# Performance work log

Hardware: AMD Instinct MI355X
Metric: run time of the kernel (lower is better)

## Reference

```python
import jax, jax.numpy as jnp
import numpy as np

N_NODES = 50000
N_EDGES = 600000
N_GRAPHS = 256
D = 128          # hidden_dim
L = 4            # num_layer
OUT = 1          # output_dim
ATOM_DIMS = [119, 5, 12, 12, 10, 6, 6, 2, 2]   # table size = dim+1, pad to 120
BOND_DIMS = [6, 6, 2, 2, 2]                    # table size = dim+1, pad to 7
BN_EPS = 1e-5


def setup_inputs() -> dict:
    key = jax.random.key(0)
    ks = jax.random.split(key, 16)
    x = jax.random.randint(ks[0], (N_NODES, 9), 0, 3)
    edge_index = jax.random.randint(ks[1], (2, N_EDGES), 0, N_NODES)
    edge_attr = jax.random.randint(ks[2], (N_EDGES, 5), 0, 3)
    batch = jnp.sort(jax.random.randint(ks[3], (N_NODES,), 0, N_GRAPHS))
    s = 0.1
    # padded atom embedding tables: [9, 120, D] (rows beyond dim+1 unused)
    atom_emb = jax.random.normal(ks[4], (9, 120, D), jnp.float32) * s
    # padded bond tables per layer: [L, 5, 7, D]
    bond_emb = jax.random.normal(ks[5], (L, 5, 7, D), jnp.float32) * s
    lin_w = jax.random.normal(ks[6], (L, D, D), jnp.float32) * (1.0 / np.sqrt(D))
    lin_b = jnp.zeros((L, D), jnp.float32)
    bn_gamma = jnp.ones((L, D), jnp.float32)
    bn_beta = jnp.zeros((L, D), jnp.float32)
    mlp_w1 = jax.random.normal(ks[7], (D // 2, D), jnp.float32) * (1.0 / np.sqrt(D))
    mlp_b1 = jnp.zeros((D // 2,), jnp.float32)
    mlp_w2 = jax.random.normal(ks[8], (OUT, D // 2), jnp.float32) * (1.0 / np.sqrt(D // 2))
    mlp_b2 = jnp.zeros((OUT,), jnp.float32)
    return dict(x=x, edge_index=edge_index, edge_attr=edge_attr, batch=batch,
                atom_emb=atom_emb, bond_emb=bond_emb, lin_w=lin_w, lin_b=lin_b,
                bn_gamma=bn_gamma, bn_beta=bn_beta,
                mlp_w1=mlp_w1, mlp_b1=mlp_b1, mlp_w2=mlp_w2, mlp_b2=mlp_b2)


def _multi_embed(tables, idx):
    # tables: [F, V, D], idx: [N, F] -> sum_f tables[f][idx[:, f]]
    return jax.vmap(lambda t, i: t[i], in_axes=(0, 1))(tables, idx).sum(0)


def reference(x, edge_index, edge_attr, batch, atom_emb, bond_emb, lin_w, lin_b,
              bn_gamma, bn_beta, mlp_w1, mlp_b1, mlp_w2, mlp_b2):
    n = x.shape[0]
    loop = jnp.arange(n, dtype=edge_index.dtype)
    src = jnp.concatenate([edge_index[0], loop])           # x_j (source)
    dst = jnp.concatenate([edge_index[1], loop])           # aggregate into target i
    ea = jnp.concatenate([edge_attr, jnp.zeros((n, 5), edge_attr.dtype)], axis=0)
    h = _multi_embed(atom_emb, x)                          # [N, D]
    for l in range(L):
        e_emb = _multi_embed(bond_emb[l], ea)              # [E+N, D]
        msg = h[src] + e_emb                               # gather + add
        aggr = jax.ops.segment_sum(msg, dst, num_segments=n)
        z = aggr @ lin_w[l].T + lin_b[l]
        mu = z.mean(0)
        var = z.var(0)                                     # biased, matches torch BN fwd
        h = jax.nn.relu((z - mu) * jax.lax.rsqrt(var + BN_EPS) * bn_gamma[l] + bn_beta[l])
    # global mean pool
    sums = jax.ops.segment_sum(h, batch, num_segments=N_GRAPHS)
    cnt = jax.ops.segment_sum(jnp.ones((n,), h.dtype), batch, num_segments=N_GRAPHS)
    g = sums / jnp.maximum(cnt, 1.0)[:, None]
    # MLP head (dropout inactive at inference)
    out = jax.nn.relu(g @ mlp_w1.T + mlp_b1) @ mlp_w2.T + mlp_b2
    return out
```

## Files before the change

### kernel.cpp

```cpp
#include <hip/hip_runtime.h>
#include <hip/hip_bf16.h>
#include <stdint.h>

#define D 128
#define NGRAPH 256
#define BN_EPS 1e-5f
#define NCOMBO 243
#define AGG_BLOCKS 512
#define AGG_THREADS 768
#define MAXDEG 48
#define GEMM_ROWS 128

typedef unsigned short u16;
typedef __attribute__((ext_vector_type(8))) short bf16x8;
typedef __attribute__((ext_vector_type(4))) float f32x4;

__device__ inline u16 f2bf(float a) {
  return __builtin_bit_cast(u16, __float2bfloat16(a));
}
__device__ inline uint32_t pk2(float a, float b) {
  return (uint32_t)f2bf(a) | ((uint32_t)f2bf(b) << 16);
}
__device__ inline float bflo(uint32_t u) { return __builtin_bit_cast(float, u << 16); }
__device__ inline float bfhi(uint32_t u) { return __builtin_bit_cast(float, u & 0xffff0000u); }
__device__ inline void unpack8(uint4 v, float* f) {
  f[0] = bflo(v.x); f[1] = bfhi(v.x); f[2] = bflo(v.y); f[3] = bfhi(v.y);
  f[4] = bflo(v.z); f[5] = bfhi(v.z); f[6] = bflo(v.w); f[7] = bfhi(v.w);
}

__global__ __launch_bounds__(256) void setup_kernel(
    const int* __restrict__ x, const float* __restrict__ atom_emb,
    float* __restrict__ h0,
    const int* __restrict__ src, const int* __restrict__ dst,
    const int* __restrict__ attr, int* __restrict__ deg,
    uint2* __restrict__ edges, int ne,
    const int* __restrict__ batch, int* __restrict__ goff,
    float* __restrict__ gsum, int n) {
  int b = blockIdx.x, tid = threadIdx.x;
  int nscat = (ne + 255) >> 8;
  int nemb = (n * 32 + 255) >> 8;
  if (b < nscat) {
    int e = b * 256 + tid;
    if (e >= ne) return;
    int d = dst[e];
    int slot = atomicAdd(&deg[d], 1);
    if (slot >= MAXDEG) return;
    int a0 = attr[e * 5 + 0], a1 = attr[e * 5 + 1], a2 = attr[e * 5 + 2];
    int a3 = attr[e * 5 + 3], a4 = attr[e * 5 + 4];
    uint32_t packed = (uint32_t)(a0 * 81 + a1 * 27 + a2 * 9 + a3 * 3 + a4);
    uint2 r; r.x = (uint32_t)src[e]; r.y = packed;
    edges[(size_t)d * MAXDEG + slot] = r;
  } else if (b < nscat + nemb) {
    int t = (b - nscat) * 256 + tid;
    int node = t >> 5, cq = t & 31;
    if (node >= n) return;
    float4 acc = {0.f, 0.f, 0.f, 0.f};
#pragma unroll
    for (int f = 0; f < 9; f++) {
      int idx = x[node * 9 + f];
      const float4* row = (const float4*)(atom_emb + ((size_t)f * 120 + idx) * D);
      float4 v = row[cq];
      acc.x += v.x; acc.y += v.y; acc.z += v.z; acc.w += v.w;
    }
    ((float4*)(h0 + (size_t)node * D))[cq] = acc;
  } else {
    if (b == nscat + nemb) {
      for (int t = tid; t < 4 * 2 * D; t += 256) gsum[t] = 0.f;
    }
    int i = (b - nscat - nemb) * 256 + tid;
    if (i >= n) return;
    int bb = batch[i];
    if (i == 0) {
      for (int g = 0; g <= bb; g++) goff[g] = 0;
    } else {
      int pb = batch[i - 1];
      for (int g = pb + 1; g <= bb; g++) goff[g] = i;
    }
    if (i == n - 1) {
      for (int g = bb + 1; g <= NGRAPH; g++) goff[g] = n;
    }
  }
}

__global__ __launch_bounds__(128) void prep_kernel(
    const float* __restrict__ bemb, const float* __restrict__ linw,
    u16* __restrict__ tabB, u16* __restrict__ wball) {
  __shared__ float row[D];
  int b = blockIdx.x, c = threadIdx.x;
  if (b < 4 * NCOMBO) {
    int l = b / NCOMBO, r = b % NCOMBO;
    const float* bond = bemb + (size_t)l * 5 * 7 * D;
    const float* W = linw + (size_t)l * D * D;
    int a0 = r / 81, a1 = (r / 27) % 3, a2 = (r / 9) % 3, a3 = (r / 3) % 3,
        a4 = r % 3;
    float v = bond[(0 * 7 + a0) * D + c] + bond[(1 * 7 + a1) * D + c] +
              bond[(2 * 7 + a2) * D + c] + bond[(3 * 7 + a3) * D + c] +
              bond[(4 * 7 + a4) * D + c];
    row[c] = v;
    __syncthreads();
    float s = 0.f;
    for (int k = 0; k < D; k++) s += row[k] * W[(size_t)c * D + k];
    tabB[((size_t)l * NCOMBO + r) * D + c] = f2bf(s);
  } else {
    int i = b - 4 * NCOMBO;
    int l = i >> 7, j = i & 127;
    float v = linw[(size_t)l * D * D + (size_t)j * D + c];
    wball[(size_t)l * D * D + (size_t)j * D + (c ^ ((j & 7) << 3))] = f2bf(v);
  }
}

__global__ __launch_bounds__(256) void gemm_kernel(const float* __restrict__ in,
                                                   const u16* __restrict__ Wb,
                                                   const float* __restrict__ gsum,
                                                   const float* __restrict__ gamma,
                                                   const float* __restrict__ beta,
                                                   float invN,
                                                   u16* __restrict__ out, int M) {
  __shared__ u16 wlds[D * D];
  __shared__ float bns[2 * D];
  int tid = threadIdx.x;
  for (int i = tid; i < D * D / 8; i += 256)
    ((uint4*)wlds)[i] = ((const uint4*)Wb)[i];
  if (gsum && tid < D) {
    float s = gsum[tid], q = gsum[D + tid];
    float mu = s * invN;
    float var = q * invN - mu * mu;
    float sc = rsqrtf(var + BN_EPS) * gamma[tid];
    bns[tid] = sc;
    bns[D + tid] = beta[tid] - mu * sc;
  }
  __syncthreads();

  int wave = tid >> 6, lane = tid & 63;
  int quad = lane >> 4, l16 = lane & 15;
  int m0 = blockIdx.x * GEMM_ROWS + wave * 32;

  f32x4 acc[2][8];
#pragma unroll
  for (int mt = 0; mt < 2; mt++)
#pragma unroll
    for (int t = 0; t < 8; t++) acc[mt][t] = (f32x4){0.f, 0.f, 0.f, 0.f};

#pragma unroll
  for (int kk = 0; kk < 4; kk++) {
    int k0 = kk * 32 + quad * 8;
    bf16x8 a[2];
#pragma unroll
    for (int mt = 0; mt < 2; mt++) {
      int m = m0 + mt * 16 + l16;
      if (m < M) {
        float4 v0 = *(const float4*)(in + (size_t)m * D + k0);
        float4 v1 = *(const float4*)(in + (size_t)m * D + k0 + 4);
        if (gsum) {
          float4 sc0 = *(const float4*)(bns + k0);
          float4 sc1 = *(const float4*)(bns + k0 + 4);
          float4 sh0 = *(const float4*)(bns + D + k0);
          float4 sh1 = *(const float4*)(bns + D + k0 + 4);
          v0.x = fmaxf(v0.x * sc0.x + sh0.x, 0.f);
          v0.y = fmaxf(v0.y * sc0.y + sh0.y, 0.f);
          v0.z = fmaxf(v0.z * sc0.z + sh0.z, 0.f);
          v0.w = fmaxf(v0.w * sc0.w + sh0.w, 0.f);
          v1.x = fmaxf(v1.x * sc1.x + sh1.x, 0.f);
          v1.y = fmaxf(v1.y * sc1.y + sh1.y, 0.f);
          v1.z = fmaxf(v1.z * sc1.z + sh1.z, 0.f);
          v1.w = fmaxf(v1.w * sc1.w + sh1.w, 0.f);
        }
        uint4 pa = {pk2(v0.x, v0.y), pk2(v0.z, v0.w), pk2(v1.x, v1.y), pk2(v1.z, v1.w)};
        a[mt] = __builtin_bit_cast(bf16x8, pa);
      } else {
        uint4 pz = {0u, 0u, 0u, 0u};
        a[mt] = __builtin_bit_cast(bf16x8, pz);
      }
    }
#pragma unroll
    for (int nt = 0; nt < 8; nt++) {
      int nrow = nt * 16 + l16;
      uint4 braw = *(const uint4*)(wlds + nrow * D + (k0 ^ ((nrow & 7) << 3)));
      bf16x8 bfrag = __builtin_bit_cast(bf16x8, braw);
      acc[0][nt] = __builtin_amdgcn_mfma_f32_16x16x32_bf16(a[0], bfrag, acc[0][nt], 0, 0, 0);
      acc[1][nt] = __builtin_amdgcn_mfma_f32_16x16x32_bf16(a[1], bfrag, acc[1][nt], 0, 0, 0);
    }
  }
#pragma unroll
  for (int mt = 0; mt < 2; mt++)
#pragma unroll
    for (int r = 0; r < 4; r++) {
      int row = m0 + mt * 16 + quad * 4 + r;
      if (row < M) {
#pragma unroll
        for (int nt = 0; nt < 8; nt++)
          out[(size_t)row * D + nt * 16 + l16] = f2bf(acc[mt][nt][r]);
      }
    }
}

__global__ __launch_bounds__(AGG_THREADS, 6) void agg_kernel(
    const u16* __restrict__ ht, const u16* __restrict__ tabT,
    const float* __restrict__ linb, const uint2* __restrict__ edges,
    const int* __restrict__ deg, float* __restrict__ z,
    float* __restrict__ gsum, int n) {
  __shared__ u16 tabs[NCOMBO * D];
  __shared__ float psum[2 * D];
  int tid = threadIdx.x;
  for (int i = tid; i < NCOMBO * D / 8; i += AGG_THREADS)
    ((uint4*)tabs)[i] = ((const uint4*)tabT)[i];
  if (tid < 2 * D) psum[tid] = 0.f;
  __syncthreads();

  int lane = tid & 63;
  int g = lane >> 4;
  int c8 = lane & 15;
  int wid = (blockIdx.x * AGG_THREADS + tid) >> 6;
  int nw = (gridDim.x * AGG_THREADS) >> 6;

  float lbz[8];
  {
    float4 l0 = ((const float4*)linb)[c8 * 2];
    float4 l1 = ((const float4*)linb)[c8 * 2 + 1];
    float t0[8];
    unpack8(*(const uint4*)(tabs + c8 * 8), t0);
    lbz[0] = l0.x + t0[0]; lbz[1] = l0.y + t0[1];
    lbz[2] = l0.z + t0[2]; lbz[3] = l0.w + t0[3];
    lbz[4] = l1.x + t0[4]; lbz[5] = l1.y + t0[5];
    lbz[6] = l1.z + t0[6]; lbz[7] = l1.w + t0[7];
  }
  float st[8];
#pragma unroll
  for (int i = 0; i < 8; i++) st[i] = 0.f;

  int dgv = (wid < n) ? deg[wid] : 0;
  for (int node = wid; node < n; node += nw) {
    int dg = dgv;
    if (node + nw < n) dgv = deg[node + nw];
    int cnt = (dg > MAXDEG) ? MAXDEG : dg;
    int base = node * MAXDEG;
    int e = base + cnt;
    int j = base + g;

    uint4 selfv;
    if (g == 0) selfv = *(const uint4*)(ht + (size_t)node * D + c8 * 8);
    bool v0 = j < e, v1 = j + 4 < e, v2 = j + 8 < e;
    uint2 rA, rB, rC;
    if (v0) rA = edges[j];
    if (v1) rB = edges[j + 4];
    if (v2) rC = edges[j + 8];
    uint4 hA, hB;
    if (v0) hA = *(const uint4*)(ht + (size_t)rA.x * D + c8 * 8);
    if (v1) hB = *(const uint4*)(ht + (size_t)rB.x * D + c8 * 8);

    float acc[8];
#pragma unroll
    for (int i = 0; i < 8; i++) acc[i] = 0.f;

    while (v0) {
      bool v3 = j + 12 < e;
      uint2 rN;
      if (v3) rN = edges[j + 12];
      uint4 hC;
      if (v2) hC = *(const uint4*)(ht + (size_t)rC.x * D + c8 * 8);
      uint4 tb = *(const uint4*)(tabs + (size_t)rA.y * D + c8 * 8);
      float hf[8], tf[8];
      unpack8(hA, hf);
      unpack8(tb, tf);
#pragma unroll
      for (int i = 0; i < 8; i++) acc[i] += hf[i] + tf[i];
      rA = rB; rB = rC; rC = rN;
      hA = hB; hB = hC;
      v0 = v1; v1 = v2; v2 = v3;
      j += 4;
    }

    if (g == 0) {
      float sv[8];
      unpack8(selfv, sv);
#pragma unroll
      for (int i = 0; i < 8; i++) acc[i] += sv[i] + lbz[i];
    }

#pragma unroll
    for (int off = 16; off <= 32; off <<= 1)
#pragma unroll
      for (int i = 0; i < 8; i++) acc[i] += __shfl_xor(acc[i], off, 64);

    if (g == 0) {
      float4 za = {acc[0], acc[1], acc[2], acc[3]};
      float4 zb4 = {acc[4], acc[5], acc[6], acc[7]};
      float4* zr = (float4*)(z + (size_t)node * D);
      zr[c8 * 2] = za;
      zr[c8 * 2 + 1] = zb4;
    } else if (g == 1) {
#pragma unroll
      for (int i = 0; i < 8; i++) st[i] += acc[i];
    } else if (g == 2) {
#pragma unroll
      for (int i = 0; i < 8; i++) st[i] += acc[i] * acc[i];
    }
  }
  {
    int c0 = c8 * 8;
    if (g == 1) {
#pragma unroll
      for (int i = 0; i < 8; i++) atomicAdd(&psum[c0 + i], st[i]);
    } else if (g == 2) {
#pragma unroll
      for (int i = 0; i < 8; i++) atomicAdd(&psum[D + c0 + i], st[i]);
    }
  }
  __syncthreads();
  if (tid < 2 * D) atomicAdd(&gsum[tid], psum[tid]);
}

__global__ __launch_bounds__(512) void poolmlp_kernel(
    const float* __restrict__ z, const float* __restrict__ gsum,
    const float* __restrict__ gamma, const float* __restrict__ beta,
    float invN, const int* __restrict__ goff,
    const float* __restrict__ w1, const float* __restrict__ b1,
    const float* __restrict__ w2, const float* __restrict__ b2,
    float* __restrict__ out) {
  __shared__ float sdata[512];
  __shared__ float pg[D];
  int g = blockIdx.x;
  int c = threadIdx.x & 127, r4 = threadIdx.x >> 7;
  float s0 = gsum[c], q0 = gsum[D + c];
  float mu = s0 * invN;
  float var = q0 * invN - mu * mu;
  float sc = rsqrtf(var + BN_EPS) * gamma[c];
  float sh = beta[c] - mu * sc;
  int s = goff[g], cnt = goff[g + 1] - s;
  float acc = 0.f;
  for (int i = r4; i < cnt; i += 4) {
    float zv = z[(size_t)(s + i) * D + c];
    acc += fmaxf(zv * sc + sh, 0.f);
  }
  sdata[threadIdx.x] = acc;
  __syncthreads();
  if (r4 == 0) {
    float t = sdata[c] + sdata[128 + c] + sdata[256 + c] + sdata[384 + c];
    pg[c] = t / fmaxf((float)cnt, 1.f);
  }
  __syncthreads();
  if (threadIdx.x < 64) {
    int j = threadIdx.x;
    float v = b1[j];
    for (int k = 0; k < D; k++) v += pg[k] * w1[(size_t)j * D + k];
    v = fmaxf(v, 0.f) * w2[j];
#pragma unroll
    for (int off = 32; off > 0; off >>= 1) v += __shfl_down(v, off, 64);
    if (j == 0) out[g] = v + b2[0];
  }
}

extern "C" void kernel_launch(void* const* d_in, const int* in_sizes, int n_in,
                              void* d_out, int out_size, void* d_ws, size_t ws_size,
                              hipStream_t stream) {
  const int*   x     = (const int*)d_in[0];
  const int*   eidx  = (const int*)d_in[1];
  const int*   eattr = (const int*)d_in[2];
  const int*   batch = (const int*)d_in[3];
  const float* aemb  = (const float*)d_in[4];
  const float* bemb  = (const float*)d_in[5];
  const float* linw  = (const float*)d_in[6];
  const float* linb  = (const float*)d_in[7];
  const float* gamma = (const float*)d_in[8];
  const float* beta  = (const float*)d_in[9];
  const float* w1    = (const float*)d_in[10];
  const float* b1    = (const float*)d_in[11];
  const float* w2    = (const float*)d_in[12];
  const float* b2    = (const float*)d_in[13];
  float* out = (float*)d_out;

  int n  = in_sizes[3];
  int ne = in_sizes[1] / 2;
  float invN = 1.f / (float)n;

  char* p = (char*)d_ws;
  auto alloc = [&](size_t bytes) {
    char* r = p;
    p += (bytes + 255) & ~(size_t)255;
    return r;
  };
  float* bufA   = (float*)alloc((size_t)n * D * 4);
  u16*   bufB   = (u16*)alloc((size_t)n * D * 2);
  uint2* edges  = (uint2*)alloc((size_t)n * MAXDEG * 8);
  int*   deg    = (int*)alloc((size_t)n * 4);
  int*   goff   = (int*)alloc((size_t)(NGRAPH + 1) * 4);
  u16*   tabB   = (u16*)alloc((size_t)4 * NCOMBO * D * 2);
  u16*   wball  = (u16*)alloc((size_t)4 * D * D * 2);
  float* gsum   = (float*)alloc((size_t)4 * 2 * D * 4);

  hipMemsetAsync(deg, 0, (size_t)n * 4, stream);

  int nscat = (ne + 255) >> 8;
  int nemb = (n * 32 + 255) >> 8;
  int ngoff = (n + 255) >> 8;
  setup_kernel<<<nscat + nemb + ngoff, 256, 0, stream>>>(
      x, aemb, bufA, eidx, eidx + ne, eattr, deg, edges, ne, batch, goff,
      gsum, n);
  prep_kernel<<<4 * NCOMBO + 4 * D, 128, 0, stream>>>(bemb, linw, tabB, wball);

  for (int l = 0; l < 4; l++) {
    gemm_kernel<<<(n + GEMM_ROWS - 1) / GEMM_ROWS, 256, 0, stream>>>(
        bufA, wball + (size_t)l * D * D,
        l ? (gsum + (size_t)(l - 1) * 2 * D) : (const float*)nullptr,
        l ? (gamma + (size_t)(l - 1) * D) : (const float*)nullptr,
        l ? (beta + (size_t)(l - 1) * D) : (const float*)nullptr,
        invN, bufB, n);
    agg_kernel<<<AGG_BLOCKS, AGG_THREADS, 0, stream>>>(
        bufB, tabB + (size_t)l * NCOMBO * D, linb + (size_t)l * D, edges, deg,
        bufA, gsum + (size_t)l * 2 * D, n);
  }
  poolmlp_kernel<<<NGRAPH, 512, 0, stream>>>(
      bufA, gsum + 3 * 2 * D, gamma + 3 * D, beta + 3 * D, invN, goff,
      w1, b1, w2, b2, out);
}
```

Measured before the change: 368.1 us.

## Store activations in bf16, pack edge records into 32 bits, widen agg blocks

```diff
diff --git a/kernel.cpp b/kernel.cpp
--- a/kernel.cpp
+++ b/kernel.cpp
@@ -7,7 +7,7 @@
 #define BN_EPS 1e-5f
 #define NCOMBO 243
 #define AGG_BLOCKS 512
-#define AGG_THREADS 768
+#define AGG_THREADS 1024
 #define MAXDEG 48
 #define GEMM_ROWS 128
 
@@ -23,6 +23,7 @@
 }
 __device__ inline float bflo(uint32_t u) { return __builtin_bit_cast(float, u << 16); }
 __device__ inline float bfhi(uint32_t u) { return __builtin_bit_cast(float, u & 0xffff0000u); }
+__device__ inline float bf1(u16 u) { return __builtin_bit_cast(float, (uint32_t)u << 16); }
 __device__ inline void unpack8(uint4 v, float* f) {
   f[0] = bflo(v.x); f[1] = bfhi(v.x); f[2] = bflo(v.y); f[3] = bfhi(v.y);
   f[4] = bflo(v.z); f[5] = bfhi(v.z); f[6] = bflo(v.w); f[7] = bfhi(v.w);
@@ -30,10 +31,10 @@
 
 __global__ __launch_bounds__(256) void setup_kernel(
     const int* __restrict__ x, const float* __restrict__ atom_emb,
-    float* __restrict__ h0,
+    u16* __restrict__ h0,
     const int* __restrict__ src, const int* __restrict__ dst,
     const int* __restrict__ attr, int* __restrict__ deg,
-    uint2* __restrict__ edges, int ne,
+    uint32_t* __restrict__ edges, int ne,
     const int* __restrict__ batch, int* __restrict__ goff,
     float* __restrict__ gsum, int n) {
   int b = blockIdx.x, tid = threadIdx.x;
@@ -47,9 +48,8 @@
     if (slot >= MAXDEG) return;
     int a0 = attr[e * 5 + 0], a1 = attr[e * 5 + 1], a2 = attr[e * 5 + 2];
     int a3 = attr[e * 5 + 3], a4 = attr[e * 5 + 4];
-    uint32_t packed = (uint32_t)(a0 * 81 + a1 * 27 + a2 * 9 + a3 * 3 + a4);
-    uint2 r; r.x = (uint32_t)src[e]; r.y = packed;
-    edges[(size_t)d * MAXDEG + slot] = r;
+    uint32_t combo = (uint32_t)(a0 * 81 + a1 * 27 + a2 * 9 + a3 * 3 + a4);
+    edges[(size_t)d * MAXDEG + slot] = (uint32_t)src[e] | (combo << 16);
   } else if (b < nscat + nemb) {
     int t = (b - nscat) * 256 + tid;
     int node = t >> 5, cq = t & 31;
@@ -62,7 +62,8 @@
       float4 v = row[cq];
       acc.x += v.x; acc.y += v.y; acc.z += v.z; acc.w += v.w;
     }
-    ((float4*)(h0 + (size_t)node * D))[cq] = acc;
+    uint2 o = {pk2(acc.x, acc.y), pk2(acc.z, acc.w)};
+    ((uint2*)(h0 + (size_t)node * D))[cq] = o;
   } else {
     if (b == nscat + nemb) {
       for (int t = tid; t < 4 * 2 * D; t += 256) gsum[t] = 0.f;
@@ -109,7 +110,7 @@
   }
 }
 
-__global__ __launch_bounds__(256) void gemm_kernel(const float* __restrict__ in,
+__global__ __launch_bounds__(256) void gemm_kernel(const u16* __restrict__ in,
                                                    const u16* __restrict__ Wb,
                                                    const float* __restrict__ gsum,
                                                    const float* __restrict__ gamma,
@@ -149,24 +150,26 @@
     for (int mt = 0; mt < 2; mt++) {
       int m = m0 + mt * 16 + l16;
       if (m < M) {
-        float4 v0 = *(const float4*)(in + (size_t)m * D + k0);
-        float4 v1 = *(const float4*)(in + (size_t)m * D + k0 + 4);
+        uint4 v = *(const uint4*)(in + (size_t)m * D + k0);
         if (gsum) {
+          float f[8];
+          unpack8(v, f);
           float4 sc0 = *(const float4*)(bns + k0);
           float4 sc1 = *(const float4*)(bns + k0 + 4);
           float4 sh0 = *(const float4*)(bns + D + k0);
           float4 sh1 = *(const float4*)(bns + D + k0 + 4);
-          v0.x = fmaxf(v0.x * sc0.x + sh0.x, 0.f);
-          v0.y = fmaxf(v0.y * sc0.y + sh0.y, 0.f);
-          v0.z = fmaxf(v0.z * sc0.z + sh0.z, 0.f);
-          v0.w = fmaxf(v0.w * sc0.w + sh0.w, 0.f);
-          v1.x = fmaxf(v1.x * sc1.x + sh1.x, 0.f);
-          v1.y = fmaxf(v1.y * sc1.y + sh1.y, 0.f);
-          v1.z = fmaxf(v1.z * sc1.z + sh1.z, 0.f);
-          v1.w = fmaxf(v1.w * sc1.w + sh1.w, 0.f);
+          f[0] = fmaxf(f[0] * sc0.x + sh0.x, 0.f);
+          f[1] = fmaxf(f[1] * sc0.y + sh0.y, 0.f);
+          f[2] = fmaxf(f[2] * sc0.z + sh0.z, 0.f);
+          f[3] = fmaxf(f[3] * sc0.w + sh0.w, 0.f);
+          f[4] = fmaxf(f[4] * sc1.x + sh1.x, 0.f);
+          f[5] = fmaxf(f[5] * sc1.y + sh1.y, 0.f);
+          f[6] = fmaxf(f[6] * sc1.z + sh1.z, 0.f);
+          f[7] = fmaxf(f[7] * sc1.w + sh1.w, 0.f);
+          v = (uint4){pk2(f[0], f[1]), pk2(f[2], f[3]),
+                      pk2(f[4], f[5]), pk2(f[6], f[7])};
         }
-        uint4 pa = {pk2(v0.x, v0.y), pk2(v0.z, v0.w), pk2(v1.x, v1.y), pk2(v1.z, v1.w)};
-        a[mt] = __builtin_bit_cast(bf16x8, pa);
+        a[mt] = __builtin_bit_cast(bf16x8, v);
       } else {
         uint4 pz = {0u, 0u, 0u, 0u};
         a[mt] = __builtin_bit_cast(bf16x8, pz);
@@ -194,10 +197,10 @@
     }
 }
 
-__global__ __launch_bounds__(AGG_THREADS, 6) void agg_kernel(
+__global__ __launch_bounds__(AGG_THREADS, 8) void agg_kernel(
     const u16* __restrict__ ht, const u16* __restrict__ tabT,
-    const float* __restrict__ linb, const uint2* __restrict__ edges,
-    const int* __restrict__ deg, float* __restrict__ z,
+    const float* __restrict__ linb, const uint32_t* __restrict__ edges,
+    const int* __restrict__ deg, u16* __restrict__ z,
     float* __restrict__ gsum, int n) {
   __shared__ u16 tabs[NCOMBO * D];
   __shared__ float psum[2 * D];
@@ -240,13 +243,13 @@
     uint4 selfv;
     if (g == 0) selfv = *(const uint4*)(ht + (size_t)node * D + c8 * 8);
     bool v0 = j < e, v1 = j + 4 < e, v2 = j + 8 < e;
-    uint2 rA, rB, rC;
+    uint32_t rA, rB, rC;
     if (v0) rA = edges[j];
     if (v1) rB = edges[j + 4];
     if (v2) rC = edges[j + 8];
     uint4 hA, hB;
-    if (v0) hA = *(const uint4*)(ht + (size_t)rA.x * D + c8 * 8);
-    if (v1) hB = *(const uint4*)(ht + (size_t)rB.x * D + c8 * 8);
+    if (v0) hA = *(const uint4*)(ht + (size_t)(rA & 0xffffu) * D + c8 * 8);
+    if (v1) hB = *(const uint4*)(ht + (size_t)(rB & 0xffffu) * D + c8 * 8);
 
     float acc[8];
 #pragma unroll
@@ -254,11 +257,11 @@
 
     while (v0) {
       bool v3 = j + 12 < e;
-      uint2 rN;
+      uint32_t rN;
       if (v3) rN = edges[j + 12];
       uint4 hC;
-      if (v2) hC = *(const uint4*)(ht + (size_t)rC.x * D + c8 * 8);
-      uint4 tb = *(const uint4*)(tabs + (size_t)rA.y * D + c8 * 8);
+      if (v2) hC = *(const uint4*)(ht + (size_t)(rC & 0xffffu) * D + c8 * 8);
+      uint4 tb = *(const uint4*)(tabs + (size_t)(rA >> 16) * D + c8 * 8);
       float hf[8], tf[8];
       unpack8(hA, hf);
       unpack8(tb, tf);
@@ -283,11 +286,9 @@
       for (int i = 0; i < 8; i++) acc[i] += __shfl_xor(acc[i], off, 64);
 
     if (g == 0) {
-      float4 za = {acc[0], acc[1], acc[2], acc[3]};
-      float4 zb4 = {acc[4], acc[5], acc[6], acc[7]};
-      float4* zr = (float4*)(z + (size_t)node * D);
-      zr[c8 * 2] = za;
-      zr[c8 * 2 + 1] = zb4;
+      uint4 zo = {pk2(acc[0], acc[1]), pk2(acc[2], acc[3]),
+                  pk2(acc[4], acc[5]), pk2(acc[6], acc[7])};
+      *(uint4*)(z + (size_t)node * D + c8 * 8) = zo;
     } else if (g == 1) {
 #pragma unroll
       for (int i = 0; i < 8; i++) st[i] += acc[i];
@@ -311,7 +312,7 @@
 }
 
 __global__ __launch_bounds__(512) void poolmlp_kernel(
-    const float* __restrict__ z, const float* __restrict__ gsum,
+    const u16* __restrict__ z, const float* __restrict__ gsum,
     const float* __restrict__ gamma, const float* __restrict__ beta,
     float invN, const int* __restrict__ goff,
     const float* __restrict__ w1, const float* __restrict__ b1,
@@ -329,7 +330,7 @@
   int s = goff[g], cnt = goff[g + 1] - s;
   float acc = 0.f;
   for (int i = r4; i < cnt; i += 4) {
-    float zv = z[(size_t)(s + i) * D + c];
+    float zv = bf1(z[(size_t)(s + i) * D + c]);
     acc += fmaxf(zv * sc + sh, 0.f);
   }
   sdata[threadIdx.x] = acc;
@@ -379,14 +380,14 @@
     p += (bytes + 255) & ~(size_t)255;
     return r;
   };
-  float* bufA   = (float*)alloc((size_t)n * D * 4);
-  u16*   bufB   = (u16*)alloc((size_t)n * D * 2);
-  uint2* edges  = (uint2*)alloc((size_t)n * MAXDEG * 8);
-  int*   deg    = (int*)alloc((size_t)n * 4);
-  int*   goff   = (int*)alloc((size_t)(NGRAPH + 1) * 4);
-  u16*   tabB   = (u16*)alloc((size_t)4 * NCOMBO * D * 2);
-  u16*   wball  = (u16*)alloc((size_t)4 * D * D * 2);
-  float* gsum   = (float*)alloc((size_t)4 * 2 * D * 4);
+  u16*      bufA   = (u16*)alloc((size_t)n * D * 2);
+  u16*      bufB   = (u16*)alloc((size_t)n * D * 2);
+  uint32_t* edges  = (uint32_t*)alloc((size_t)n * MAXDEG * 4);
+  int*      deg    = (int*)alloc((size_t)n * 4);
+  int*      goff   = (int*)alloc((size_t)(NGRAPH + 1) * 4);
+  u16*      tabB   = (u16*)alloc((size_t)4 * NCOMBO * D * 2);
+  u16*      wball  = (u16*)alloc((size_t)4 * D * D * 2);
+  float*    gsum   = (float*)alloc((size_t)4 * 2 * D * 4);
 
   hipMemsetAsync(deg, 0, (size_t)n * 4, stream);
 
```

After: 457.9 us. 1.24x slower.
